# Kernel tuning notes

Hardware: AMD Instinct MI355X
Metric: run time of the kernel (lower is better)

The kernel has to match this reference:

```python
import jax, jax.numpy as jnp
import numpy as np

B, F, T, EPT, S, E, H, LVL = 16384, 512, 4, 2, 2, 256, 128, 2

def _ple_level(xs_task, x_sh, w_task, b_task, w_sh, b_sh, w_gate, b_gate, w_gsh=None, b_gsh=None):
    # xs_task: [T,B,I] per-task inputs; x_sh: [B,I] shared input
    task_out = jax.nn.relu(jnp.einsum('tbi,teio->tbeo', xs_task, w_task) + b_task[:, None])  # [T,B,EPT,E]
    sh_out = jax.nn.relu(jnp.einsum('bi,sio->bso', x_sh, w_sh) + b_sh)                       # [B,S,E]
    t = task_out.shape[0]
    experts = jnp.concatenate([task_out, jnp.broadcast_to(sh_out[None], (t,) + sh_out.shape)], axis=2)  # [T,B,EPT+S,E]
    gate = jax.nn.softmax(jnp.einsum('tbi,tig->tbg', xs_task, w_gate) + b_gate[:, None], axis=-1)
    task_next = jnp.einsum('tbg,tbge->tbe', gate, experts)  # [T,B,E]
    sh_next = None
    if w_gsh is not None:
        # all experts ordered task0_exp0, task0_exp1, task1_exp0, ..., then shared
        bsz = x_sh.shape[0]
        all_exp = jnp.concatenate([jnp.transpose(task_out, (1, 0, 2, 3)).reshape(bsz, -1, task_out.shape[-1]), sh_out], axis=1)
        gsh = jax.nn.softmax(x_sh @ w_gsh + b_gsh, axis=-1)
        sh_next = jnp.einsum('bg,bge->be', gsh, all_exp)
    return task_next, sh_next

def setup_inputs() -> dict:
    key = jax.random.key(0)
    ks = jax.random.split(key, 16)
    sc = 0.02
    d = {
        'x': jax.random.normal(ks[0], (B, F), jnp.float32),
        # level 0 (in_dim=F, has shared gate)
        'w_task0': jax.random.normal(ks[1], (T, EPT, F, E), jnp.float32) * sc,
        'b_task0': jnp.zeros((T, EPT, E), jnp.float32),
        'w_sh0': jax.random.normal(ks[2], (S, F, E), jnp.float32) * sc,
        'b_sh0': jnp.zeros((S, E), jnp.float32),
        'w_gate0': jax.random.normal(ks[3], (T, F, EPT + S), jnp.float32) * sc,
        'b_gate0': jnp.zeros((T, EPT + S), jnp.float32),
        'w_gsh0': jax.random.normal(ks[4], (F, T * EPT + S), jnp.float32) * sc,
        'b_gsh0': jnp.zeros((T * EPT + S,), jnp.float32),
        # level 1 (last; in_dim=E, no shared gate)
        'w_task1': jax.random.normal(ks[5], (T, EPT, E, E), jnp.float32) * sc,
        'b_task1': jnp.zeros((T, EPT, E), jnp.float32),
        'w_sh1': jax.random.normal(ks[6], (S, E, E), jnp.float32) * sc,
        'b_sh1': jnp.zeros((S, E), jnp.float32),
        'w_gate1': jax.random.normal(ks[7], (T, E, EPT + S), jnp.float32) * sc,
        'b_gate1': jnp.zeros((T, EPT + S), jnp.float32),
        # towers
        'w_tw': jax.random.normal(ks[8], (T, E, H), jnp.float32) * sc,
        'b_tw': jnp.zeros((T, H), jnp.float32),
        'w_out': jax.random.normal(ks[9], (T, H, 2), jnp.float32) * sc,
        'b_out': jnp.zeros((T, 2), jnp.float32),
    }
    return d

def reference(x, w_task0, b_task0, w_sh0, b_sh0, w_gate0, b_gate0, w_gsh0, b_gsh0,
              w_task1, b_task1, w_sh1, b_sh1, w_gate1, b_gate1,
              w_tw, b_tw, w_out, b_out):
    xs_task = jnp.broadcast_to(x[None], (T,) + x.shape)  # all tasks see same input at level 0
    t1, sh1 = _ple_level(xs_task, x, w_task0, b_task0, w_sh0, b_sh0, w_gate0, b_gate0, w_gsh0, b_gsh0)
    t2, _ = _ple_level(t1, sh1, w_task1, b_task1, w_sh1, b_sh1, w_gate1, b_gate1)
    h = jax.nn.relu(jnp.einsum('tbe,teh->tbh', t2, w_tw) + b_tw[:, None])
    logits = jnp.einsum('tbh,tho->tbo', h, w_out) + b_out[:, None]
    p = jax.nn.softmax(logits, axis=-1)
    return jnp.clip(p, 1e-15, 1.0 - 1e-15)  # [T,B,2]
```

## Files before the change

### kernel.cpp

```cpp
#include <hip/hip_runtime.h>

typedef unsigned short u16;
typedef __bf16 bf16x8 __attribute__((ext_vector_type(8)));
typedef float f32x4 __attribute__((ext_vector_type(4)));
typedef u16 u16x8 __attribute__((ext_vector_type(8)));

#define B_ 16384
#define XR(r) ((((r) & 3) ^ (((r) >> 2) & 3)))

__device__ __forceinline__ u16 f2b(float f){
  unsigned u = __builtin_bit_cast(unsigned, f);
  u = (u + 0x7FFFu + ((u >> 16) & 1u)) >> 16;
  return (u16)u;
}
__device__ __forceinline__ float b2f(u16 v){
  return __builtin_bit_cast(float, ((unsigned)v) << 16);
}
__device__ __forceinline__ void ld8(const u16* __restrict__ p, float* f){
  u16x8 v = *(const u16x8*)p;
  #pragma unroll
  for (int j = 0; j < 8; ++j) f[j] = b2f(v[j]);
}
__device__ __forceinline__ void st8(u16* __restrict__ p, const float* f){
  u16x8 v;
  #pragma unroll
  for (int j = 0; j < 8; ++j) v[j] = f2b(f[j]);
  *(u16x8*)p = v;
}

__device__ __forceinline__ void gload16(const u16* g, u16* lds){
  __builtin_amdgcn_global_load_lds(
      (const __attribute__((address_space(1))) unsigned int*)g,
      (__attribute__((address_space(3))) unsigned int*)lds, 16, 0, 0);
}

__device__ __forceinline__ void gemm_core2(const u16* __restrict__ A,
                                           const u16* __restrict__ Wt,
                                           int K, int m0, int n0, int nt,
                                           u16* sm, f32x4 acc[4][4])
{
  const int tid  = threadIdx.x;
  const int lane = tid & 63;
  const int wm   = ((tid >> 7) & 3) * 64;
  const int wn   = ((tid >> 6) & 1) * 64;

  f32x4 zero = {0.f, 0.f, 0.f, 0.f};
  #pragma unroll
  for (int mi = 0; mi < 4; ++mi)
    #pragma unroll
    for (int ni = 0; ni < 4; ++ni) acc[mi][ni] = zero;

  const int rA0 = tid >> 2, rA1 = 128 + (tid >> 2), rB = tid >> 2;
  const u16* gA0 = A  + (size_t)(m0 + rA0) * K + (((tid & 3) ^ XR(rA0)) * 8);
  const u16* gA1 = A  + (size_t)(m0 + rA1) * K + (((tid & 3) ^ XR(rA1)) * 8);
  const u16* gB  = Wt + (size_t)(n0 + rB ) * K + (((tid & 3) ^ XR(rB )) * 8);
  const int wbase = (tid >> 6) * 512;

  int aoff[4], boff[4];
  #pragma unroll
  for (int m = 0; m < 4; ++m) {
    int r = wm + m * 16 + (lane & 15);
    aoff[m] = r * 32 + (((lane >> 4) ^ XR(r)) * 8);
  }
  #pragma unroll
  for (int n = 0; n < 4; ++n) {
    int r = wn + n * 16 + (lane & 15);
    boff[n] = r * 32 + (((lane >> 4) ^ XR(r)) * 8);
  }

  #pragma unroll
  for (int j = 0; j < 2; ++j) {
    u16* sl = sm + j * 12288;
    gload16(gA0 + j * 32, sl + wbase);
    gload16(gA1 + j * 32, sl + 4096 + wbase);
    gload16(gB  + j * 32, sl + 8192 + wbase);
  }
  asm volatile("s_waitcnt vmcnt(3)" ::: "memory");
  __builtin_amdgcn_s_barrier();

  int cs = 0;
  for (int j = 0; j < nt; ++j) {
    if (j + 2 < nt) {
      int ns = cs + 2; ns = (ns >= 3) ? ns - 3 : ns;
      u16* sl = sm + ns * 12288;
      gload16(gA0 + (size_t)(j + 2) * 32, sl + wbase);
      gload16(gA1 + (size_t)(j + 2) * 32, sl + 4096 + wbase);
      gload16(gB  + (size_t)(j + 2) * 32, sl + 8192 + wbase);
    }
    const u16* sa = sm + cs * 12288;
    const u16* sb = sa + 8192;
    bf16x8 av[4], bv[4];
    #pragma unroll
    for (int m = 0; m < 4; ++m) av[m] = *(const bf16x8*)(sa + aoff[m]);
    #pragma unroll
    for (int n = 0; n < 4; ++n) bv[n] = *(const bf16x8*)(sb + boff[n]);
    #pragma unroll
    for (int m = 0; m < 4; ++m)
      #pragma unroll
      for (int n = 0; n < 4; ++n)
        acc[m][n] = __builtin_amdgcn_mfma_f32_16x16x32_bf16(av[m], bv[n], acc[m][n], 0, 0, 0);
    if (j + 2 < nt)      asm volatile("s_waitcnt vmcnt(3)" ::: "memory");
    else if (j + 1 < nt) asm volatile("s_waitcnt vmcnt(0)" ::: "memory");
    __builtin_amdgcn_s_barrier();
    cs = (cs == 2) ? 0 : cs + 1;
  }
}


__global__ __launch_bounds__(512) void k_gemm0(const u16* __restrict__ xb,
    const u16* __restrict__ Wt0, const float* __restrict__ bias0,
    u16* __restrict__ E0, float* __restrict__ G0L)
{
  __shared__ __align__(16) u16 sm[36864];
  f32x4 acc[4][4];
  const int bid = blockIdx.x;
  const int swz = (bid & 7) * 168 + (bid >> 3);
  const int m0 = (swz / 21) * 256, n0 = (swz % 21) * 128;
  gemm_core2(xb, Wt0, 512, m0, n0, 16, sm, acc);
  const int lane = threadIdx.x & 63;
  const int wm = ((threadIdx.x >> 7) & 3) * 64, wn = ((threadIdx.x >> 6) & 1) * 64;
  #pragma unroll
  for (int mi = 0; mi < 4; ++mi)
    #pragma unroll
    for (int ni = 0; ni < 4; ++ni) {
      int gcol = n0 + wn + ni * 16 + (lane & 15);
      float bias = bias0[gcol];
      #pragma unroll
      for (int r = 0; r < 4; ++r) {
        int grow = m0 + wm + mi * 16 + ((lane >> 4) << 2) + r;
        float v = acc[mi][ni][r] + bias;
        if (gcol < 2560)      E0[(size_t)grow * 2560 + gcol] = f2b(fmaxf(v, 0.f));
        else if (gcol < 2586) G0L[(size_t)grow * 26 + (gcol - 2560)] = v;
      }
    }
}

__global__ __launch_bounds__(256) void k_mix0(const u16* __restrict__ E0,
    const float* __restrict__ G0L, u16* __restrict__ T1SH)
{
  const int b = blockIdx.x * 8 + (threadIdx.x >> 5);
  const int e0 = (threadIdx.x & 31) * 8;
  const float* gl = G0L + (size_t)b * 26;
  float g[4][4];
  #pragma unroll
  for (int t = 0; t < 4; ++t) {
    float l0 = gl[t*4+0], l1 = gl[t*4+1], l2 = gl[t*4+2], l3 = gl[t*4+3];
    float m = fmaxf(fmaxf(l0, l1), fmaxf(l2, l3));
    float e0e = expf(l0-m), e1 = expf(l1-m), e2 = expf(l2-m), e3 = expf(l3-m);
    float inv = 1.f / (e0e + e1 + e2 + e3);
    g[t][0] = e0e*inv; g[t][1] = e1*inv; g[t][2] = e2*inv; g[t][3] = e3*inv;
  }
  float gs[10];
  {
    float m = gl[16];
    #pragma unroll
    for (int j = 1; j < 10; ++j) m = fmaxf(m, gl[16 + j]);
    float s = 0.f;
    #pragma unroll
    for (int j = 0; j < 10; ++j) { gs[j] = expf(gl[16 + j] - m); s += gs[j]; }
    float inv = 1.f / s;
    #pragma unroll
    for (int j = 0; j < 10; ++j) gs[j] *= inv;
  }
  const u16* row = E0 + (size_t)b * 2560;
  float sh0[8], sh1[8], shacc[8];
  ld8(row + 2048 + e0, sh0);
  ld8(row + 2304 + e0, sh1);
  #pragma unroll
  for (int j = 0; j < 8; ++j) shacc[j] = gs[8]*sh0[j] + gs[9]*sh1[j];
  #pragma unroll
  for (int t = 0; t < 4; ++t) {
    float te0[8], te1[8], v[8];
    ld8(row + (t*2+0)*256 + e0, te0);
    ld8(row + (t*2+1)*256 + e0, te1);
    #pragma unroll
    for (int j = 0; j < 8; ++j) {
      v[j] = g[t][0]*te0[j] + g[t][1]*te1[j] + g[t][2]*sh0[j] + g[t][3]*sh1[j];
      shacc[j] += gs[t*2+0]*te0[j] + gs[t*2+1]*te1[j];
    }
    st8(T1SH + ((size_t)t * B_ + b) * 256 + e0, v);
  }
  st8(T1SH + ((size_t)4 * B_ + b) * 256 + e0, shacc);
}

__global__ __launch_bounds__(512) void k_gemm1(const u16* __restrict__ T1SH,
    const u16* __restrict__ Wt1, const float* __restrict__ bias1,
    u16* __restrict__ E1, float* __restrict__ G1L, u16* __restrict__ SH1E)
{
  const int z = blockIdx.z;
  const int m0 = blockIdx.x * 256, n0 = blockIdx.y * 128;
  if (z == 4 && n0 >= 512) return;
  __shared__ __align__(16) u16 sm[36864];
  f32x4 acc[4][4];
  gemm_core2(T1SH + (size_t)z * B_ * 256, Wt1 + (size_t)z * 640 * 256, 256, m0, n0, 8, sm, acc);
  const int lane = threadIdx.x & 63;
  const int wm = ((threadIdx.x >> 7) & 3) * 64, wn = ((threadIdx.x >> 6) & 1) * 64;
  const float* bias = bias1 + z * 640;
  #pragma unroll
  for (int mi = 0; mi < 4; ++mi)
    #pragma unroll
    for (int ni = 0; ni < 4; ++ni) {
      int gcol = n0 + wn + ni * 16 + (lane & 15);
      float bv = bias[gcol];
      #pragma unroll
      for (int r = 0; r < 4; ++r) {
        int grow = m0 + wm + mi * 16 + ((lane >> 4) << 2) + r;
        float v = acc[mi][ni][r] + bv;
        if (z < 4) {
          if (gcol < 512)      E1[((size_t)z * B_ + grow) * 512 + gcol] = f2b(fmaxf(v, 0.f));
          else if (gcol < 516) G1L[((size_t)z * B_ + grow) * 4 + (gcol - 512)] = v;
        } else {
          if (gcol < 512)      SH1E[(size_t)grow * 512 + gcol] = f2b(fmaxf(v, 0.f));
        }
      }
    }
}

__global__ __launch_bounds__(256) void k_mix1(const u16* __restrict__ E1,
    const float* __restrict__ G1L, const u16* __restrict__ SH1E, u16* __restrict__ T2)
{
  const int b = blockIdx.x * 8 + (threadIdx.x >> 5);
  const int e0 = (threadIdx.x & 31) * 8;
  float sh0[8], sh1[8];
  ld8(SH1E + (size_t)b * 512 + e0, sh0);
  ld8(SH1E + (size_t)b * 512 + 256 + e0, sh1);
  #pragma unroll
  for (int t = 0; t < 4; ++t) {
    const float* gl = G1L + ((size_t)t * B_ + b) * 4;
    float l0 = gl[0], l1 = gl[1], l2 = gl[2], l3 = gl[3];
    float m = fmaxf(fmaxf(l0, l1), fmaxf(l2, l3));
    float x0 = expf(l0-m), x1 = expf(l1-m), x2 = expf(l2-m), x3 = expf(l3-m);
    float inv = 1.f / (x0 + x1 + x2 + x3);
    float g0 = x0*inv, g1 = x1*inv, g2 = x2*inv, g3 = x3*inv;
    float te0[8], te1[8], v[8];
    ld8(E1 + ((size_t)t * B_ + b) * 512 + e0, te0);
    ld8(E1 + ((size_t)t * B_ + b) * 512 + 256 + e0, te1);
    #pragma unroll
    for (int j = 0; j < 8; ++j)
      v[j] = g0*te0[j] + g1*te1[j] + g2*sh0[j] + g3*sh1[j];
    st8(T2 + ((size_t)t * B_ + b) * 256 + e0, v);
  }
}

__global__ __launch_bounds__(512) void k_tower(const u16* __restrict__ T2,
    const u16* __restrict__ Wtw, const float* __restrict__ b_tw,
    const float* __restrict__ w_out, const float* __restrict__ b_out,
    float* __restrict__ out)
{
  __shared__ __align__(16) u16 sm[36864];
  __shared__ float part[2][256][2];
  f32x4 acc[4][4];
  const int z = blockIdx.z;
  const int m0 = blockIdx.x * 256;
  gemm_core2(T2 + (size_t)z * B_ * 256, Wtw + (size_t)z * 128 * 256, 256, m0, 0, 8, sm, acc);
  const int lane = threadIdx.x & 63;
  const int wm = ((threadIdx.x >> 7) & 3) * 64, wn = ((threadIdx.x >> 6) & 1) * 64;
  #pragma unroll
  for (int mi = 0; mi < 4; ++mi) {
    #pragma unroll
    for (int r = 0; r < 4; ++r) {
      float p0 = 0.f, p1 = 0.f;
      #pragma unroll
      for (int ni = 0; ni < 4; ++ni) {
        int col = wn + ni * 16 + (lane & 15);
        float h = fmaxf(acc[mi][ni][r] + b_tw[z * 128 + col], 0.f);
        p0 += h * w_out[(z * 128 + col) * 2 + 0];
        p1 += h * w_out[(z * 128 + col) * 2 + 1];
      }
      #pragma unroll
      for (int off = 1; off < 16; off <<= 1) {
        p0 += __shfl_xor(p0, off);
        p1 += __shfl_xor(p1, off);
      }
      if ((lane & 15) == 0) {
        int rowl = wm + mi * 16 + ((lane >> 4) << 2) + r;
        part[(threadIdx.x >> 6) & 1][rowl][0] = p0;
        part[(threadIdx.x >> 6) & 1][rowl][1] = p1;
      }
    }
  }
  __syncthreads();
  if (threadIdx.x < 256) {
    int rowl = threadIdx.x;
    float l0 = part[0][rowl][0] + part[1][rowl][0] + b_out[z * 2 + 0];
    float l1 = part[0][rowl][1] + part[1][rowl][1] + b_out[z * 2 + 1];
    float mx = fmaxf(l0, l1);
    float e0 = expf(l0 - mx), e1 = expf(l1 - mx);
    float inv = 1.f / (e0 + e1);
    float p0 = fminf(fmaxf(e0 * inv, 1e-15f), 1.0f);
    float p1 = fminf(fmaxf(e1 * inv, 1e-15f), 1.0f);
    size_t o = ((size_t)z * B_ + m0 + rowl) * 2;
    out[o] = p0; out[o + 1] = p1;
  }
}

__global__ void k_prep(const float* __restrict__ x,
    const float* __restrict__ w_task0, const float* __restrict__ b_task0,
    const float* __restrict__ w_sh0,   const float* __restrict__ b_sh0,
    const float* __restrict__ w_gate0, const float* __restrict__ b_gate0,
    const float* __restrict__ w_gsh0,  const float* __restrict__ b_gsh0,
    const float* __restrict__ w_task1, const float* __restrict__ b_task1,
    const float* __restrict__ w_sh1,   const float* __restrict__ b_sh1,
    const float* __restrict__ w_gate1, const float* __restrict__ b_gate1,
    const float* __restrict__ w_tw,
    u16* __restrict__ xb, u16* __restrict__ Wt0, float* __restrict__ bias0,
    u16* __restrict__ Wt1, float* __restrict__ bias1, u16* __restrict__ Wtw)
{
  size_t i = (size_t)blockIdx.x * 256 + threadIdx.x;
  const size_t S_X8  = (size_t)16384 * 512 / 8;
  const size_t S_WT0 = (size_t)2688 * 512;
  const size_t S_B0  = 2688;
  const size_t S_WT1 = (size_t)5 * 640 * 256;
  const size_t S_B1  = 5 * 640;
  const size_t S_WTW = (size_t)4 * 128 * 256;

  if (i < S_X8) {
    size_t o = i * 8;
    float4 a = *(const float4*)(x + o);
    float4 b = *(const float4*)(x + o + 4);
    u16x8 v;
    v[0] = f2b(a.x); v[1] = f2b(a.y); v[2] = f2b(a.z); v[3] = f2b(a.w);
    v[4] = f2b(b.x); v[5] = f2b(b.y); v[6] = f2b(b.z); v[7] = f2b(b.w);
    *(u16x8*)(xb + o) = v;
    return;
  }
  i -= S_X8;
  if (i < S_WT0) {
    int c = (int)(i / 512), f = (int)(i % 512);
    float v = 0.f;
    if (c < 2048)      { int te = c >> 8, o = c & 255; v = w_task0[((size_t)te * 512 + f) * 256 + o]; }
    else if (c < 2560) { int s = (c - 2048) >> 8, o = c & 255; v = w_sh0[((size_t)s * 512 + f) * 256 + o]; }
    else if (c < 2576) { int q = c - 2560; int t = q >> 2, gg = q & 3; v = w_gate0[((size_t)t * 512 + f) * 4 + gg]; }
    else if (c < 2586) { int j = c - 2576; v = w_gsh0[(size_t)f * 10 + j]; }
    Wt0[i] = f2b(v);
    return;
  }
  i -= S_WT0;
  if (i < S_B0) {
    int c = (int)i; float v = 0.f;
    if (c < 2048)      { int te = c >> 8, o = c & 255; v = b_task0[te * 256 + o]; }
    else if (c < 2560) { int s = (c - 2048) >> 8, o = c & 255; v = b_sh0[s * 256 + o]; }
    else if (c < 2576) { v = b_gate0[c - 2560]; }
    else if (c < 2586) { v = b_gsh0[c - 2576]; }
    bias0[c] = v;
    return;
  }
  i -= S_B0;
  if (i < S_WT1) {
    int z = (int)(i / (640 * 256)); int rem = (int)(i % (640 * 256));
    int c = rem / 256, f = rem % 256;
    float v = 0.f;
    if (z < 4) {
      if (c < 512)      { int ee = c >> 8, o = c & 255; v = w_task1[(((size_t)(z * 2 + ee)) * 256 + f) * 256 + o]; }
      else if (c < 516) { int gg = c - 512; v = w_gate1[((size_t)z * 256 + f) * 4 + gg]; }
    } else {
      if (c < 512)      { int s = c >> 8, o = c & 255; v = w_sh1[((size_t)s * 256 + f) * 256 + o]; }
    }
    Wt1[i] = f2b(v);
    return;
  }
  i -= S_WT1;
  if (i < S_B1) {
    int z = (int)(i / 640); int c = (int)(i % 640);
    float v = 0.f;
    if (z < 4) {
      if (c < 512)      { int ee = c >> 8, o = c & 255; v = b_task1[(z * 2 + ee) * 256 + o]; }
      else if (c < 516) { v = b_gate1[z * 4 + (c - 512)]; }
    } else {
      if (c < 512)      { int s = c >> 8, o = c & 255; v = b_sh1[s * 256 + o]; }
    }
    bias1[(size_t)z * 640 + c] = v;
    return;
  }
  i -= S_B1;
  if (i < S_WTW) {
    int z = (int)(i / (128 * 256)); int rem = (int)(i % (128 * 256));
    int h = rem / 256, f = rem % 256;
    Wtw[i] = f2b(w_tw[((size_t)z * 256 + f) * 128 + h]);
    return;
  }
}

extern "C" void kernel_launch(void* const* d_in, const int* in_sizes, int n_in,
                              void* d_out, int out_size, void* d_ws, size_t ws_size,
                              hipStream_t stream)
{
  (void)in_sizes; (void)n_in; (void)out_size; (void)ws_size;
  const float* x       = (const float*)d_in[0];
  const float* w_task0 = (const float*)d_in[1];
  const float* b_task0 = (const float*)d_in[2];
  const float* w_sh0   = (const float*)d_in[3];
  const float* b_sh0   = (const float*)d_in[4];
  const float* w_gate0 = (const float*)d_in[5];
  const float* b_gate0 = (const float*)d_in[6];
  const float* w_gsh0  = (const float*)d_in[7];
  const float* b_gsh0  = (const float*)d_in[8];
  const float* w_task1 = (const float*)d_in[9];
  const float* b_task1 = (const float*)d_in[10];
  const float* w_sh1   = (const float*)d_in[11];
  const float* b_sh1   = (const float*)d_in[12];
  const float* w_gate1 = (const float*)d_in[13];
  const float* b_gate1 = (const float*)d_in[14];
  const float* w_tw    = (const float*)d_in[15];
  const float* b_tw    = (const float*)d_in[16];
  const float* w_out   = (const float*)d_in[17];
  const float* b_out   = (const float*)d_in[18];
  float* out = (float*)d_out;

  char* ws = (char*)d_ws;
  u16*   XB    = (u16*)  (ws + 0);
  u16*   WT0   = (u16*)  (ws + 16777216);
  float* BIAS0 = (float*)(ws + 19529728);
  u16*   WT1   = (u16*)  (ws + 19540480);
  float* BIAS1 = (float*)(ws + 21178880);
  u16*   WTW   = (u16*)  (ws + 21191680);
  u16*   E0    = (u16*)  (ws + 21453824);
  float* G0L   = (float*)(ws + 105339904);
  u16*   T1SH  = (u16*)  (ws + 107043840);
  u16*   E1    = (u16*)  (ws + 148986880);
  float* G1L   = (float*)(ws + 216095744);
  u16*   SH1E  = (u16*)  (ws + 217144320);
  u16*   T2    = (u16*)  (ws + 21453824);

  k_prep<<<13207, 256, 0, stream>>>(x, w_task0, b_task0, w_sh0, b_sh0, w_gate0, b_gate0,
      w_gsh0, b_gsh0, w_task1, b_task1, w_sh1, b_sh1, w_gate1, b_gate1, w_tw,
      XB, WT0, BIAS0, WT1, BIAS1, WTW);
  k_gemm0<<<1344, 512, 0, stream>>>(XB, WT0, BIAS0, E0, G0L);
  k_mix0<<<2048, 256, 0, stream>>>(E0, G0L, T1SH);
  k_gemm1<<<dim3(64, 5, 5), 512, 0, stream>>>(T1SH, WT1, BIAS1, E1, G1L, SH1E);
  k_mix1<<<2048, 256, 0, stream>>>(E1, G1L, SH1E, T2);
  k_tower<<<dim3(64, 1, 4), 512, 0, stream>>>(T2, WTW, b_tw, w_out, b_out, out);
}
```

Before: 181.5 us.

## Double the GEMM K-tile to 64 with an 8-way XOR swizzle

The shared GEMM core now stages 64-wide K slices instead of 32 per pipeline stage. Each wave issues six 16-byte async loads per stage over a new row-of-8 mapping, and LDS reads use an 8-way XOR swizzle. This halves the number of loop iterations and barriers per GEMM and runs two MFMA k-steps per barrier. In exchange, LDS use per block doubles to 144KB across three stages, which may limit occupancy to one block per CU.

```diff
diff --git a/kernel.cpp b/kernel.cpp
--- a/kernel.cpp
+++ b/kernel.cpp
@@ -6,7 +6,6 @@
 typedef u16 u16x8 __attribute__((ext_vector_type(8)));
 
 #define B_ 16384
-#define XR(r) ((((r) & 3) ^ (((r) >> 2) & 3)))
 
 __device__ __forceinline__ u16 f2b(float f){
   unsigned u = __builtin_bit_cast(unsigned, f);
@@ -34,13 +33,14 @@
       (__attribute__((address_space(3))) unsigned int*)lds, 16, 0, 0);
 }
 
-__device__ __forceinline__ void gemm_core2(const u16* __restrict__ A,
+__device__ __forceinline__ void gemm_core3(const u16* __restrict__ A,
                                            const u16* __restrict__ Wt,
                                            int K, int m0, int n0, int nt,
                                            u16* sm, f32x4 acc[4][4])
 {
   const int tid  = threadIdx.x;
   const int lane = tid & 63;
+  const int wave = tid >> 6;
   const int wm   = ((tid >> 7) & 3) * 64;
   const int wn   = ((tid >> 6) & 1) * 64;
 
@@ -50,56 +50,69 @@
     #pragma unroll
     for (int ni = 0; ni < 4; ++ni) acc[mi][ni] = zero;
 
-  const int rA0 = tid >> 2, rA1 = 128 + (tid >> 2), rB = tid >> 2;
-  const u16* gA0 = A  + (size_t)(m0 + rA0) * K + (((tid & 3) ^ XR(rA0)) * 8);
-  const u16* gA1 = A  + (size_t)(m0 + rA1) * K + (((tid & 3) ^ XR(rA1)) * 8);
-  const u16* gB  = Wt + (size_t)(n0 + rB ) * K + (((tid & 3) ^ XR(rB )) * 8);
-  const int wbase = (tid >> 6) * 512;
-
-  int aoff[4], boff[4];
-  #pragma unroll
-  for (int m = 0; m < 4; ++m) {
-    int r = wm + m * 16 + (lane & 15);
-    aoff[m] = r * 32 + (((lane >> 4) ^ XR(r)) * 8);
-  }
-  #pragma unroll
-  for (int n = 0; n < 4; ++n) {
-    int r = wn + n * 16 + (lane & 15);
-    boff[n] = r * 32 + (((lane >> 4) ^ XR(r)) * 8);
+  const int srow  = lane >> 3;
+  const int gslot = (lane & 7) ^ srow;
+  const u16* gsrc[6];
+  int gdst[6];
+  #pragma unroll
+  for (int i = 0; i < 6; ++i) {
+    int c = wave * 6 + i;
+    if (c < 32) {
+      gsrc[i] = A + (size_t)(m0 + c * 8 + srow) * K + gslot * 8;
+      gdst[i] = c * 512;
+    } else {
+      gsrc[i] = Wt + (size_t)(n0 + (c - 32) * 8 + srow) * K + gslot * 8;
+      gdst[i] = 16384 + (c - 32) * 512;
+    }
+  }
+
+  int aoff[2][4], boff[2][4];
+  #pragma unroll
+  for (int kk = 0; kk < 2; ++kk) {
+    #pragma unroll
+    for (int m = 0; m < 4; ++m) {
+      int r = wm + m * 16 + (lane & 15);
+      aoff[kk][m] = r * 64 + (((kk * 4 + (lane >> 4)) ^ (r & 7)) * 8);
+    }
+    #pragma unroll
+    for (int n = 0; n < 4; ++n) {
+      int r = wn + n * 16 + (lane & 15);
+      boff[kk][n] = 16384 + r * 64 + (((kk * 4 + (lane >> 4)) ^ (r & 7)) * 8);
+    }
   }
 
   #pragma unroll
   for (int j = 0; j < 2; ++j) {
-    u16* sl = sm + j * 12288;
-    gload16(gA0 + j * 32, sl + wbase);
-    gload16(gA1 + j * 32, sl + 4096 + wbase);
-    gload16(gB  + j * 32, sl + 8192 + wbase);
-  }
-  asm volatile("s_waitcnt vmcnt(3)" ::: "memory");
+    u16* base = sm + j * 24576;
+    #pragma unroll
+    for (int i = 0; i < 6; ++i) gload16(gsrc[i] + j * 64, base + gdst[i]);
+  }
+  asm volatile("s_waitcnt vmcnt(6)" ::: "memory");
   __builtin_amdgcn_s_barrier();
 
   int cs = 0;
   for (int j = 0; j < nt; ++j) {
     if (j + 2 < nt) {
       int ns = cs + 2; ns = (ns >= 3) ? ns - 3 : ns;
-      u16* sl = sm + ns * 12288;
-      gload16(gA0 + (size_t)(j + 2) * 32, sl + wbase);
-      gload16(gA1 + (size_t)(j + 2) * 32, sl + 4096 + wbase);
-      gload16(gB  + (size_t)(j + 2) * 32, sl + 8192 + wbase);
-    }
-    const u16* sa = sm + cs * 12288;
-    const u16* sb = sa + 8192;
-    bf16x8 av[4], bv[4];
-    #pragma unroll
-    for (int m = 0; m < 4; ++m) av[m] = *(const bf16x8*)(sa + aoff[m]);
-    #pragma unroll
-    for (int n = 0; n < 4; ++n) bv[n] = *(const bf16x8*)(sb + boff[n]);
-    #pragma unroll
-    for (int m = 0; m < 4; ++m)
-      #pragma unroll
-      for (int n = 0; n < 4; ++n)
-        acc[m][n] = __builtin_amdgcn_mfma_f32_16x16x32_bf16(av[m], bv[n], acc[m][n], 0, 0, 0);
-    if (j + 2 < nt)      asm volatile("s_waitcnt vmcnt(3)" ::: "memory");
+      u16* base = sm + ns * 24576;
+      #pragma unroll
+      for (int i = 0; i < 6; ++i) gload16(gsrc[i] + (size_t)(j + 2) * 64, base + gdst[i]);
+    }
+    const u16* sa = sm + cs * 24576;
+    #pragma unroll
+    for (int kk = 0; kk < 2; ++kk) {
+      bf16x8 av[4], bv[4];
+      #pragma unroll
+      for (int m = 0; m < 4; ++m) av[m] = *(const bf16x8*)(sa + aoff[kk][m]);
+      #pragma unroll
+      for (int n = 0; n < 4; ++n) bv[n] = *(const bf16x8*)(sa + boff[kk][n]);
+      #pragma unroll
+      for (int m = 0; m < 4; ++m)
+        #pragma unroll
+        for (int n = 0; n < 4; ++n)
+          acc[m][n] = __builtin_amdgcn_mfma_f32_16x16x32_bf16(av[m], bv[n], acc[m][n], 0, 0, 0);
+    }
+    if (j + 2 < nt)      asm volatile("s_waitcnt vmcnt(6)" ::: "memory");
     else if (j + 1 < nt) asm volatile("s_waitcnt vmcnt(0)" ::: "memory");
     __builtin_amdgcn_s_barrier();
     cs = (cs == 2) ? 0 : cs + 1;
@@ -111,12 +124,12 @@
     const u16* __restrict__ Wt0, const float* __restrict__ bias0,
     u16* __restrict__ E0, float* __restrict__ G0L)
 {
-  __shared__ __align__(16) u16 sm[36864];
+  __shared__ __align__(16) u16 sm[73728];
   f32x4 acc[4][4];
   const int bid = blockIdx.x;
   const int swz = (bid & 7) * 168 + (bid >> 3);
   const int m0 = (swz / 21) * 256, n0 = (swz % 21) * 128;
-  gemm_core2(xb, Wt0, 512, m0, n0, 16, sm, acc);
+  gemm_core3(xb, Wt0, 512, m0, n0, 8, sm, acc);
   const int lane = threadIdx.x & 63;
   const int wm = ((threadIdx.x >> 7) & 3) * 64, wn = ((threadIdx.x >> 6) & 1) * 64;
   #pragma unroll
@@ -190,9 +203,9 @@
   const int z = blockIdx.z;
   const int m0 = blockIdx.x * 256, n0 = blockIdx.y * 128;
   if (z == 4 && n0 >= 512) return;
-  __shared__ __align__(16) u16 sm[36864];
+  __shared__ __align__(16) u16 sm[73728];
   f32x4 acc[4][4];
-  gemm_core2(T1SH + (size_t)z * B_ * 256, Wt1 + (size_t)z * 640 * 256, 256, m0, n0, 8, sm, acc);
+  gemm_core3(T1SH + (size_t)z * B_ * 256, Wt1 + (size_t)z * 640 * 256, 256, m0, n0, 4, sm, acc);
   const int lane = threadIdx.x & 63;
   const int wm = ((threadIdx.x >> 7) & 3) * 64, wn = ((threadIdx.x >> 6) & 1) * 64;
   const float* bias = bias1 + z * 640;
@@ -247,12 +260,12 @@
     const float* __restrict__ w_out, const float* __restrict__ b_out,
     float* __restrict__ out)
 {
-  __shared__ __align__(16) u16 sm[36864];
+  __shared__ __align__(16) u16 sm[73728];
   __shared__ float part[2][256][2];
   f32x4 acc[4][4];
   const int z = blockIdx.z;
   const int m0 = blockIdx.x * 256;
-  gemm_core2(T2 + (size_t)z * B_ * 256, Wtw + (size_t)z * 128 * 256, 256, m0, 0, 8, sm, acc);
+  gemm_core3(T2 + (size_t)z * B_ * 256, Wtw + (size_t)z * 128 * 256, 256, m0, 0, 4, sm, acc);
   const int lane = threadIdx.x & 63;
   const int wm = ((threadIdx.x >> 7) & 3) * 64, wn = ((threadIdx.x >> 6) & 1) * 64;
   #pragma unroll
```

New measurement: 213.0 us. 17.4% more time.
